# Kernel optimization log

Measured on AMD Instinct MI355X. Metric: run time of the kernel, lower is better.

## Reference

```python
import jax, jax.numpy as jnp
import numpy as np

IMG = 1024       # original image resolution implied by (1024 - 1) normalization
STRIDE = 16
TEMP = 0.1
EPS = 1e-12      # F.normalize eps


def setup_inputs() -> dict:
    key = jax.random.key(0)
    k1, k2, k3, k4, k5 = jax.random.split(key, 5)
    B, C, Hf, Wf, N = 32, 256, 64, 64, 128
    feats_src = jax.random.normal(k1, (B, C, Hf, Wf), dtype=jnp.float32)
    feats_trg = jax.random.normal(k2, (B, C, Hf, Wf), dtype=jnp.float32)
    kps_src = jax.random.uniform(k3, (B, N, 2), dtype=jnp.float32) * (IMG - 1)
    kps_trg = jax.random.uniform(k4, (B, N, 2), dtype=jnp.float32) * (IMG - 1)
    kps_mask = jax.random.randint(k5, (B, N), 0, 2, dtype=jnp.int32)
    return {"feats_src": feats_src, "feats_trg": feats_trg,
            "kps_src": kps_src, "kps_trg": kps_trg, "kps_mask": kps_mask}


def _l2norm_c(x):
    # F.normalize(x, dim=1): x / max(||x||_2, eps) along channel dim
    n = jnp.sqrt(jnp.sum(x * x, axis=1, keepdims=True))
    return x / jnp.maximum(n, EPS)


def _bilinear_sample(feats, kps):
    # feats: [B,C,Hf,Wf]; kps: [B,N,2] pixel coords in [0, IMG-1]
    # Equivalent to F.grid_sample(align_corners=True, bilinear) with
    # grid = kps/(IMG-1)*2-1 -> pixel coords kps/(IMG-1)*(size-1).
    B, C, Hf, Wf = feats.shape
    x = kps[..., 0] / (IMG - 1) * (Wf - 1)  # [B,N]
    y = kps[..., 1] / (IMG - 1) * (Hf - 1)
    x0 = jnp.clip(jnp.floor(x), 0, Wf - 1).astype(jnp.int32)
    y0 = jnp.clip(jnp.floor(y), 0, Hf - 1).astype(jnp.int32)
    x1 = jnp.clip(x0 + 1, 0, Wf - 1)
    y1 = jnp.clip(y0 + 1, 0, Hf - 1)
    fx = x - x0.astype(x.dtype)
    fy = y - y0.astype(y.dtype)
    ft = jnp.transpose(feats, (0, 2, 3, 1))      # [B,Hf,Wf,C]
    bb = jnp.arange(B)[:, None]                  # [B,1] broadcasts to [B,N]
    g = lambda yy, xx: ft[bb, yy, xx]            # [B,N,C]
    wa = ((1 - fx) * (1 - fy))[..., None]
    wb = ((1 - fx) * fy)[..., None]
    wc = (fx * (1 - fy))[..., None]
    wd = (fx * fy)[..., None]
    return wa * g(y0, x0) + wb * g(y1, x0) + wc * g(y0, x1) + wd * g(y1, x1)


def reference(feats_src, feats_trg, kps_src, kps_trg, kps_mask):
    B, C, Hf, Wf = feats_src.shape
    N = kps_src.shape[1]
    fs = _l2norm_c(feats_src)
    ftg = _l2norm_c(feats_trg)

    # Query features sampled at source keypoints: [B,N,C]
    q = _bilinear_sample(fs, kps_src)

    # Logits over all target spatial positions: [B,N,Hf*Wf]
    trg_flat = ftg.reshape(B, C, Hf * Wf)
    logits = jnp.einsum('bnc,bcm->bnm', q, trg_flat) / TEMP

    # Bilinear soft targets at target keypoints (feature-grid coords)
    gx = kps_trg[..., 0] / STRIDE
    gy = kps_trg[..., 1] / STRIDE
    x0 = jnp.clip(jnp.floor(gx), 0, Wf - 1).astype(jnp.int32)
    x1 = jnp.clip(x0 + 1, 0, Wf - 1)
    y0 = jnp.clip(jnp.floor(gy), 0, Hf - 1).astype(jnp.int32)
    y1 = jnp.clip(y0 + 1, 0, Hf - 1)
    x0f, x1f = x0.astype(gx.dtype), x1.astype(gx.dtype)
    y0f, y1f = y0.astype(gy.dtype), y1.astype(gy.dtype)
    wa = (x1f - gx) * (y1f - gy)
    wb = (x1f - gx) * (gy - y0f)
    wc = (gx - x0f) * (y1f - gy)
    wd = (gx - x0f) * (gy - y0f)

    m = (kps_mask != 0).astype(logits.dtype)     # [B,N]
    w = jnp.stack([wa, wb, wc, wd], axis=-1) * m[..., None]   # [B,N,4]
    idx = jnp.stack([y0 * Wf + x0, y1 * Wf + x0,
                     y0 * Wf + x1, y1 * Wf + x1], axis=-1)    # [B,N,4]
    bb = jnp.arange(B)[:, None, None]
    nn = jnp.arange(N)[None, :, None]
    soft_targets = jnp.zeros_like(logits).at[bb, nn, idx].add(w)

    log_probs = jax.nn.log_softmax(logits, axis=-1)
    loss = -(soft_targets * log_probs).sum(axis=-1)           # [B,N]
    denom = jnp.maximum(m.sum(), 1.0)
    return (loss * m).sum() / denom
```

## Files before the change

### kernel.cpp

```cpp
#include <hip/hip_runtime.h>
#include <math.h>

#define B_    32
#define C_    256
#define HF    64
#define WF    64
#define M_    4096
#define N_    128
#define IMGM1 1023.0f
#define TEMP_ 0.1f
#define EPS_  1e-12f
#define NCH   32
#define SAS   40

typedef __attribute__((ext_vector_type(8))) short short8;
typedef __attribute__((ext_vector_type(4))) float floatx4;

__device__ __forceinline__ unsigned short f2bf(float x) {
  unsigned int u = __float_as_uint(x);
  u += 0x7fffu + ((u >> 16) & 1u);
  return (unsigned short)(u >> 16);
}
__device__ __forceinline__ float bf2f(unsigned short h) {
  return __uint_as_float(((unsigned int)h) << 16);
}
__device__ __forceinline__ float wave_sum(float v) {
#pragma unroll
  for (int off = 32; off; off >>= 1) v += __shfl_down(v, off, 64);
  return v;
}

__device__ __forceinline__ void src_geom(float kx, float ky, int& x0, int& y0,
                                         int& x1, int& y1, float& fx, float& fy) {
  const float x = kx / IMGM1 * (float)(WF - 1);
  const float y = ky / IMGM1 * (float)(HF - 1);
  x0 = (int)fminf(fmaxf(floorf(x), 0.f), 63.f);
  y0 = (int)fminf(fmaxf(floorf(y), 0.f), 63.f);
  x1 = min(x0 + 1, 63);
  y1 = min(y0 + 1, 63);
  fx = x - (float)x0;
  fy = y - (float)y0;
}

__global__ __launch_bounds__(256) void k1a_stage(const float* __restrict__ fs,
                                                 const float* __restrict__ kps,
                                                 ushort* __restrict__ corner,
                                                 float* __restrict__ ssqg) {
  const int cg = blockIdx.x, b = blockIdx.y, t = threadIdx.x;
  const int c0 = cg * 2;
  __shared__ __align__(16) float plane[2 * M_];
  __shared__ float4 ssq2[256];

  const float4* src = (const float4*)(fs + ((size_t)(b * C_ + c0)) * M_);
  float4* dst = (float4*)plane;
#pragma unroll
  for (int i = 0; i < 8; i++) dst[t + 256 * i] = src[t + 256 * i];
  __syncthreads();

  const int n = t & 127, p = t >> 7;
  const int c = c0 + p;
  const float kx = kps[((size_t)b * N_ + n) * 2 + 0];
  const float ky = kps[((size_t)b * N_ + n) * 2 + 1];
  int x0, y0, x1, y1; float fx, fy;
  src_geom(kx, ky, x0, y0, x1, y1, fx, fy);

  const float* pl = plane + p * M_;
  const float f00 = pl[y0 * WF + x0];
  const float f10 = pl[y1 * WF + x0];
  const float f01 = pl[y0 * WF + x1];
  const float f11 = pl[y1 * WF + x1];

  ushort4 cr;
  cr.x = f2bf(f00); cr.y = f2bf(f10); cr.z = f2bf(f01); cr.w = f2bf(f11);
  *(ushort4*)&corner[(((size_t)b * C_ + c) * N_ + n) * 4] = cr;

  ssq2[t] = make_float4(f00 * f00, f10 * f10, f01 * f01, f11 * f11);
  __syncthreads();
  if (t < 128) {
    const float4 a = ssq2[t], bq = ssq2[t + 128];
    float* g = ssqg + ((size_t)b * N_ + t) * 4;
    atomicAdd(g + 0, a.x + bq.x);
    atomicAdd(g + 1, a.y + bq.y);
    atomicAdd(g + 2, a.z + bq.z);
    atomicAdd(g + 3, a.w + bq.w);
  }
}

__global__ __launch_bounds__(256) void k1b_combine(const ushort* __restrict__ corner,
                                                   const float* __restrict__ ssqg,
                                                   const float* __restrict__ kps,
                                                   ushort* __restrict__ qbf) {
  const int n = blockIdx.x, b = blockIdx.y, c = threadIdx.x;
  const float kx = kps[((size_t)b * N_ + n) * 2 + 0];
  const float ky = kps[((size_t)b * N_ + n) * 2 + 1];
  int x0, y0, x1, y1; float fx, fy;
  src_geom(kx, ky, x0, y0, x1, y1, fx, fy);
  const float wa = (1.f - fx) * (1.f - fy), wb = (1.f - fx) * fy;
  const float wc = fx * (1.f - fy), wd = fx * fy;

  const float4 sq = *(const float4*)&ssqg[((size_t)b * N_ + n) * 4];
  const float r0 = 1.f / fmaxf(sqrtf(sq.x), EPS_);
  const float r1 = 1.f / fmaxf(sqrtf(sq.y), EPS_);
  const float r2 = 1.f / fmaxf(sqrtf(sq.z), EPS_);
  const float r3 = 1.f / fmaxf(sqrtf(sq.w), EPS_);

  const ushort4 cr = *(const ushort4*)&corner[(((size_t)b * C_ + c) * N_ + n) * 4];
  const float qv = wa * bf2f(cr.x) * r0 + wb * bf2f(cr.y) * r1 +
                   wc * bf2f(cr.z) * r2 + wd * bf2f(cr.w) * r3;
  qbf[((size_t)b * N_ + n) * C_ + c] = f2bf(qv);
}

__global__ __launch_bounds__(256) void k2_mfma(const float* __restrict__ trg,
                                               const ushort* __restrict__ qbf,
                                               const float* __restrict__ kps_trg,
                                               const int* __restrict__ mask,
                                               float2* __restrict__ part,
                                               float* __restrict__ tacc) {
  const int t = threadIdx.x;
  const int mb = blockIdx.x, b = blockIdx.y;
  const int m0 = mb * 128;
  const int wave = t >> 6, lane = t & 63;
  const int wn = wave >> 1, wm = wave & 1;
  const int lg = lane >> 4, ln = lane & 15;

  __shared__ __align__(16) short sA[128 * SAS];
  __shared__ __align__(16) short sB[128 * SAS];
  __shared__ __align__(16) float ssqp[16 * 128];
  __shared__ float scl[128];
  __shared__ float2 lser[128 * 2];
  __shared__ __align__(16) int   tidx[128][4];
  __shared__ __align__(16) float tw[128][4];

  floatx4 acc[4][4];
#pragma unroll
  for (int i = 0; i < 4; i++)
#pragma unroll
    for (int j = 0; j < 4; j++) acc[i][j] = (floatx4)0.f;

  float ssq[8];
#pragma unroll
  for (int e = 0; e < 8; e++) ssq[e] = 0.f;

  const ushort* qb = qbf + (size_t)b * N_ * C_;
  const float*  tb = trg + (size_t)b * C_ * M_ + m0;
  const int kk  = 2 * (t >> 4);
  const int m8  = (t & 15) * 8;
  const int gB  = kk >> 3;
  const int kin = kk & 7;

  for (int k0 = 0; k0 < C_; k0 += 32) {
#pragma unroll
    for (int l2 = 0; l2 < 2; l2++) {
      const int flat = t + 256 * l2;
      const int an = flat >> 2, ag = flat & 3;
      const short8 v = *(const short8*)(qb + an * C_ + k0 + ag * 8);
      *(short8*)&sA[an * SAS + ag * 8] = v;
    }
    {
      const float* p0 = tb + (size_t)(k0 + kk) * M_ + m8;
      const float* p1 = p0 + M_;
      const float4 a0 = *(const float4*)p0, a1 = *(const float4*)(p0 + 4);
      const float4 b0 = *(const float4*)p1, b1 = *(const float4*)(p1 + 4);
      const float v0[8] = {a0.x, a0.y, a0.z, a0.w, a1.x, a1.y, a1.z, a1.w};
      const float v1[8] = {b0.x, b0.y, b0.z, b0.w, b1.x, b1.y, b1.z, b1.w};
#pragma unroll
      for (int e = 0; e < 8; e++) {
        ssq[e] += v0[e] * v0[e] + v1[e] * v1[e];
        const int m = m8 + e;
        const int fm = (m >> 3) & 3;
        const unsigned int pr = (unsigned int)f2bf(v0[e]) | ((unsigned int)f2bf(v1[e]) << 16);
        *(unsigned int*)&sB[m * SAS + ((gB ^ fm) << 3) + kin] = pr;
      }
    }
    __syncthreads();
    short8 af[4], bfr[4];
#pragma unroll
    for (int i = 0; i < 4; i++)
      af[i] = *(const short8*)&sA[(wn * 64 + i * 16 + ln) * SAS + (lg << 3)];
#pragma unroll
    for (int j = 0; j < 4; j++) {
      const int m = wm * 64 + j * 16 + ln;
      const int fm = (m >> 3) & 3;
      bfr[j] = *(const short8*)&sB[m * SAS + ((lg ^ fm) << 3)];
    }
#pragma unroll
    for (int i = 0; i < 4; i++)
#pragma unroll
      for (int j = 0; j < 4; j++)
        acc[i][j] = __builtin_amdgcn_mfma_f32_16x16x32_bf16(af[i], bfr[j], acc[i][j], 0, 0, 0);
    __syncthreads();
  }

  *(float4*)&ssqp[(t >> 4) * 128 + m8]     = make_float4(ssq[0], ssq[1], ssq[2], ssq[3]);
  *(float4*)&ssqp[(t >> 4) * 128 + m8 + 4] = make_float4(ssq[4], ssq[5], ssq[6], ssq[7]);
  __syncthreads();
  if (t < 128) {
    float s = 0.f;
#pragma unroll
    for (int g = 0; g < 16; g++) s += ssqp[g * 128 + t];
    scl[t] = 1.f / (fmaxf(sqrtf(s), EPS_) * TEMP_);
    const float kx = kps_trg[((size_t)b * N_ + t) * 2 + 0];
    const float ky = kps_trg[((size_t)b * N_ + t) * 2 + 1];
    const float gx = kx * (1.f / 16.f), gy = ky * (1.f / 16.f);
    const int x0 = (int)fminf(fmaxf(floorf(gx), 0.f), 63.f);
    const int y0 = (int)fminf(fmaxf(floorf(gy), 0.f), 63.f);
    const int x1 = min(x0 + 1, 63), y1 = min(y0 + 1, 63);
    const float x0f = (float)x0, x1f = (float)x1, y0f = (float)y0, y1f = (float)y1;
    const float mk = (mask[(size_t)b * N_ + t] != 0) ? 1.f : 0.f;
    tidx[t][0] = y0 * WF + x0; tw[t][0] = (x1f - gx) * (y1f - gy) * mk;
    tidx[t][1] = y1 * WF + x0; tw[t][1] = (x1f - gx) * (gy - y0f) * mk;
    tidx[t][2] = y0 * WF + x1; tw[t][2] = (gx - x0f) * (y1f - gy) * mk;
    tidx[t][3] = y1 * WF + x1; tw[t][3] = (gx - x0f) * (gy - y0f) * mk;
  }
  __syncthreads();

  float scj[4];
#pragma unroll
  for (int j = 0; j < 4; j++) scj[j] = scl[wm * 64 + j * 16 + ln];
#pragma unroll
  for (int i = 0; i < 4; i++)
#pragma unroll
    for (int j = 0; j < 4; j++) acc[i][j] *= scj[j];

#pragma unroll
  for (int i = 0; i < 4; i++) {
#pragma unroll
    for (int r = 0; r < 4; r++) {
      float mx = fmaxf(fmaxf(acc[i][0][r], acc[i][1][r]), fmaxf(acc[i][2][r], acc[i][3][r]));
#pragma unroll
      for (int msk = 1; msk < 16; msk <<= 1) mx = fmaxf(mx, __shfl_xor(mx, msk, 64));
      float sm = __expf(acc[i][0][r] - mx) + __expf(acc[i][1][r] - mx) +
                 __expf(acc[i][2][r] - mx) + __expf(acc[i][3][r] - mx);
#pragma unroll
      for (int msk = 1; msk < 16; msk <<= 1) sm += __shfl_xor(sm, msk, 64);
      if (ln == 0) lser[(wn * 64 + i * 16 + lg * 4 + r) * 2 + wm] = make_float2(mx, sm);

      const int n = wn * 64 + i * 16 + lg * 4 + r;
      const int4  id4 = *(const int4*)&tidx[n][0];
      const float4 w4 = *(const float4*)&tw[n][0];
      const int   ida[4] = {id4.x, id4.y, id4.z, id4.w};
      const float wwa[4] = {w4.x, w4.y, w4.z, w4.w};
#pragma unroll
      for (int j = 0; j < 4; j++) {
        const int mg = m0 + wm * 64 + j * 16 + ln;
        const float lv = acc[i][j][r];
#pragma unroll
        for (int cc = 0; cc < 4; cc++)
          if (ida[cc] == mg && wwa[cc] != 0.f)
            atomicAdd(&tacc[(size_t)b * N_ + n], wwa[cc] * lv);
      }
    }
  }
  __syncthreads();
  if (t < 128) {
    const float2 u = lser[t * 2 + 0], v = lser[t * 2 + 1];
    const float M = fmaxf(u.x, v.x);
    const float S = u.y * __expf(u.x - M) + v.y * __expf(v.x - M);
    part[((size_t)b * N_ + t) * NCH + mb] = make_float2(M, S);
  }
}

__global__ __launch_bounds__(128) void k4_comb(const float2* __restrict__ part,
                                               const float* __restrict__ tacc,
                                               const float* __restrict__ kps_trg,
                                               const int* __restrict__ mask,
                                               float* __restrict__ gs) {
  const int b = blockIdx.x, t = threadIdx.x;
  const float2* p = part + ((size_t)b * N_ + t) * NCH;
  float M = -INFINITY;
#pragma unroll 8
  for (int c = 0; c < NCH; c++) M = fmaxf(M, p[c].x);
  float S = 0.f;
#pragma unroll 8
  for (int c = 0; c < NCH; c++) S += p[c].y * __expf(p[c].x - M);
  const float lse = M + logf(S);

  const float kx = kps_trg[((size_t)b * N_ + t) * 2 + 0];
  const float ky = kps_trg[((size_t)b * N_ + t) * 2 + 1];
  const float gx = kx * (1.f / 16.f), gy = ky * (1.f / 16.f);
  const int x0 = (int)fminf(fmaxf(floorf(gx), 0.f), 63.f);
  const int y0 = (int)fminf(fmaxf(floorf(gy), 0.f), 63.f);
  const int x1 = min(x0 + 1, 63), y1 = min(y0 + 1, 63);
  const float mk = (mask[(size_t)b * N_ + t] != 0) ? 1.f : 0.f;
  const float wsum = (float)(x1 - x0) * (float)(y1 - y0) * mk;

  float loss = wsum * lse - tacc[(size_t)b * N_ + t];
  float cnt = mk;
  loss = wave_sum(loss);
  cnt = wave_sum(cnt);
  __shared__ float sl[2], sc2[2];
  if ((t & 63) == 0) { sl[t >> 6] = loss; sc2[t >> 6] = cnt; }
  __syncthreads();
  if (t == 0) {
    atomicAdd(&gs[0], sl[0] + sl[1]);
    atomicAdd(&gs[1], sc2[0] + sc2[1]);
  }
}

__global__ void k5_final(const float* __restrict__ gs, float* __restrict__ out) {
  out[0] = gs[0] / fmaxf(gs[1], 1.f);
}

extern "C" void kernel_launch(void* const* d_in, const int* in_sizes, int n_in,
                              void* d_out, int out_size, void* d_ws, size_t ws_size,
                              hipStream_t stream) {
  const float* feats_src = (const float*)d_in[0];
  const float* feats_trg = (const float*)d_in[1];
  const float* kps_src   = (const float*)d_in[2];
  const float* kps_trg   = (const float*)d_in[3];
  const int*   kps_mask  = (const int*)d_in[4];
  float* out = (float*)d_out;

  char* wsb = (char*)d_ws;
  float*  ssqg   = (float*)(wsb + 0);
  float*  tacc   = (float*)(wsb + 65536);
  float*  gs     = (float*)(wsb + 81920);
  ushort* corner = (ushort*)(wsb + 82432);
  ushort* qbf    = (ushort*)(wsb + 8471040);
  float2* part   = (float2*)(wsb + 10568192);

  hipMemsetAsync(wsb, 0, 81928, stream);

  k1a_stage<<<dim3(C_ / 2, B_), 256, 0, stream>>>(feats_src, kps_src, corner, ssqg);
  k1b_combine<<<dim3(N_, B_), 256, 0, stream>>>(corner, ssqg, kps_src, qbf);
  k2_mfma<<<dim3(NCH, B_), 256, 0, stream>>>(feats_trg, qbf, kps_trg, kps_mask, part, tacc);
  k4_comb<<<dim3(B_), 128, 0, stream>>>(part, tacc, kps_trg, kps_mask, gs);
  k5_final<<<1, 1, 0, stream>>>(gs, out);
}
```

Baseline: 347.5 us.

## Coalesce combine kernel via LDS transpose and skip irrelevant target-scatter checks

The combine kernel now processes 32 channels by all 128 keypoints per block. It precomputes the per-keypoint weight times inverse norm once in shared memory, reads corner data contiguously, and transposes through LDS so the bf16 query writes go out as coalesced ushort4 stores instead of strided per-channel reads. The MFMA kernel also builds a per-keypoint bitmask of which 128-column chunks hold nonzero target corners, so warps skip the compare and atomic loop for chunks they cannot touch. This costs extra shared memory and a sync, and it assumes the 4096/128 = 32 chunks fit in a 32-bit mask.

```diff
diff --git a/kernel.cpp b/kernel.cpp
--- a/kernel.cpp
+++ b/kernel.cpp
@@ -86,28 +86,54 @@
   }
 }
 
-__global__ __launch_bounds__(256) void k1b_combine(const ushort* __restrict__ corner,
-                                                   const float* __restrict__ ssqg,
-                                                   const float* __restrict__ kps,
-                                                   ushort* __restrict__ qbf) {
-  const int n = blockIdx.x, b = blockIdx.y, c = threadIdx.x;
-  const float kx = kps[((size_t)b * N_ + n) * 2 + 0];
-  const float ky = kps[((size_t)b * N_ + n) * 2 + 1];
-  int x0, y0, x1, y1; float fx, fy;
-  src_geom(kx, ky, x0, y0, x1, y1, fx, fy);
-  const float wa = (1.f - fx) * (1.f - fy), wb = (1.f - fx) * fy;
-  const float wc = fx * (1.f - fy), wd = fx * fy;
-
-  const float4 sq = *(const float4*)&ssqg[((size_t)b * N_ + n) * 4];
-  const float r0 = 1.f / fmaxf(sqrtf(sq.x), EPS_);
-  const float r1 = 1.f / fmaxf(sqrtf(sq.y), EPS_);
-  const float r2 = 1.f / fmaxf(sqrtf(sq.z), EPS_);
-  const float r3 = 1.f / fmaxf(sqrtf(sq.w), EPS_);
-
-  const ushort4 cr = *(const ushort4*)&corner[(((size_t)b * C_ + c) * N_ + n) * 4];
-  const float qv = wa * bf2f(cr.x) * r0 + wb * bf2f(cr.y) * r1 +
-                   wc * bf2f(cr.z) * r2 + wd * bf2f(cr.w) * r3;
-  qbf[((size_t)b * N_ + n) * C_ + c] = f2bf(qv);
+__global__ __launch_bounds__(256) void k1b2_combine(const ushort* __restrict__ corner,
+                                                    const float* __restrict__ ssqg,
+                                                    const float* __restrict__ kps,
+                                                    ushort* __restrict__ qbf) {
+  const int cg = blockIdx.x, b = blockIdx.y, t = threadIdx.x;
+  __shared__ float4 uw[128];
+  __shared__ ushort sQ[32][137];
+
+  if (t < 128) {
+    const int n = t;
+    const float kx = kps[((size_t)b * N_ + n) * 2 + 0];
+    const float ky = kps[((size_t)b * N_ + n) * 2 + 1];
+    int x0, y0, x1, y1; float fx, fy;
+    src_geom(kx, ky, x0, y0, x1, y1, fx, fy);
+    const float wa = (1.f - fx) * (1.f - fy), wb = (1.f - fx) * fy;
+    const float wc = fx * (1.f - fy), wd = fx * fy;
+    const float4 sq = *(const float4*)&ssqg[((size_t)b * N_ + n) * 4];
+    const float r0 = 1.f / fmaxf(sqrtf(sq.x), EPS_);
+    const float r1 = 1.f / fmaxf(sqrtf(sq.y), EPS_);
+    const float r2 = 1.f / fmaxf(sqrtf(sq.z), EPS_);
+    const float r3 = 1.f / fmaxf(sqrtf(sq.w), EPS_);
+    uw[n] = make_float4(wa * r0, wb * r1, wc * r2, wd * r3);
+  }
+  __syncthreads();
+
+  const ushort* cb = corner + (((size_t)b * C_ + cg * 32) * N_) * 4;
+#pragma unroll
+  for (int i = 0; i < 16; i++) {
+    const int e = t + 256 * i;
+    const int n = e & 127, cl = e >> 7;
+    const ushort4 cr = *(const ushort4*)&cb[((size_t)cl * N_ + n) * 4];
+    const float4 u = uw[n];
+    const float qv = u.x * bf2f(cr.x) + u.y * bf2f(cr.y) +
+                     u.z * bf2f(cr.z) + u.w * bf2f(cr.w);
+    sQ[cl][n] = f2bf(qv);
+  }
+  __syncthreads();
+
+  ushort* qb = qbf + (size_t)b * N_ * C_ + cg * 32;
+#pragma unroll
+  for (int i = 0; i < 4; i++) {
+    const int o = t + 256 * i;
+    const int n = o >> 3, c4 = (o & 7) * 4;
+    ushort4 w4;
+    w4.x = sQ[c4 + 0][n]; w4.y = sQ[c4 + 1][n];
+    w4.z = sQ[c4 + 2][n]; w4.w = sQ[c4 + 3][n];
+    *(ushort4*)&qb[(size_t)n * C_ + c4] = w4;
+  }
 }
 
 __global__ __launch_bounds__(256) void k2_mfma(const float* __restrict__ trg,
@@ -130,6 +156,7 @@
   __shared__ float2 lser[128 * 2];
   __shared__ __align__(16) int   tidx[128][4];
   __shared__ __align__(16) float tw[128][4];
+  __shared__ unsigned tmask[128];
 
   floatx4 acc[4][4];
 #pragma unroll
@@ -207,10 +234,22 @@
     const int x1 = min(x0 + 1, 63), y1 = min(y0 + 1, 63);
     const float x0f = (float)x0, x1f = (float)x1, y0f = (float)y0, y1f = (float)y1;
     const float mk = (mask[(size_t)b * N_ + t] != 0) ? 1.f : 0.f;
-    tidx[t][0] = y0 * WF + x0; tw[t][0] = (x1f - gx) * (y1f - gy) * mk;
-    tidx[t][1] = y1 * WF + x0; tw[t][1] = (x1f - gx) * (gy - y0f) * mk;
-    tidx[t][2] = y0 * WF + x1; tw[t][2] = (gx - x0f) * (y1f - gy) * mk;
-    tidx[t][3] = y1 * WF + x1; tw[t][3] = (gx - x0f) * (gy - y0f) * mk;
+    const int i0 = y0 * WF + x0, i1 = y1 * WF + x0;
+    const int i2 = y0 * WF + x1, i3 = y1 * WF + x1;
+    const float w0 = (x1f - gx) * (y1f - gy) * mk;
+    const float w1 = (x1f - gx) * (gy - y0f) * mk;
+    const float w2 = (gx - x0f) * (y1f - gy) * mk;
+    const float w3 = (gx - x0f) * (gy - y0f) * mk;
+    tidx[t][0] = i0; tw[t][0] = w0;
+    tidx[t][1] = i1; tw[t][1] = w1;
+    tidx[t][2] = i2; tw[t][2] = w2;
+    tidx[t][3] = i3; tw[t][3] = w3;
+    unsigned tm = 0u;
+    if (w0 != 0.f) tm |= 1u << (i0 >> 7);
+    if (w1 != 0.f) tm |= 1u << (i1 >> 7);
+    if (w2 != 0.f) tm |= 1u << (i2 >> 7);
+    if (w3 != 0.f) tm |= 1u << (i3 >> 7);
+    tmask[t] = tm;
   }
   __syncthreads();
 
@@ -222,6 +261,7 @@
 #pragma unroll
     for (int j = 0; j < 4; j++) acc[i][j] *= scj[j];
 
+  const unsigned mbbit = 1u << mb;
 #pragma unroll
   for (int i = 0; i < 4; i++) {
 #pragma unroll
@@ -236,18 +276,20 @@
       if (ln == 0) lser[(wn * 64 + i * 16 + lg * 4 + r) * 2 + wm] = make_float2(mx, sm);
 
       const int n = wn * 64 + i * 16 + lg * 4 + r;
-      const int4  id4 = *(const int4*)&tidx[n][0];
-      const float4 w4 = *(const float4*)&tw[n][0];
-      const int   ida[4] = {id4.x, id4.y, id4.z, id4.w};
-      const float wwa[4] = {w4.x, w4.y, w4.z, w4.w};
-#pragma unroll
-      for (int j = 0; j < 4; j++) {
-        const int mg = m0 + wm * 64 + j * 16 + ln;
-        const float lv = acc[i][j][r];
-#pragma unroll
-        for (int cc = 0; cc < 4; cc++)
-          if (ida[cc] == mg && wwa[cc] != 0.f)
-            atomicAdd(&tacc[(size_t)b * N_ + n], wwa[cc] * lv);
+      if (tmask[n] & mbbit) {
+        const int4  id4 = *(const int4*)&tidx[n][0];
+        const float4 w4 = *(const float4*)&tw[n][0];
+        const int   ida[4] = {id4.x, id4.y, id4.z, id4.w};
+        const float wwa[4] = {w4.x, w4.y, w4.z, w4.w};
+#pragma unroll
+        for (int j = 0; j < 4; j++) {
+          const int mg = m0 + wm * 64 + j * 16 + ln;
+          const float lv = acc[i][j][r];
+#pragma unroll
+          for (int cc = 0; cc < 4; cc++)
+            if (ida[cc] == mg && wwa[cc] != 0.f)
+              atomicAdd(&tacc[(size_t)b * N_ + n], wwa[cc] * lv);
+        }
       }
     }
   }
@@ -322,7 +364,7 @@
   hipMemsetAsync(wsb, 0, 81928, stream);
 
   k1a_stage<<<dim3(C_ / 2, B_), 256, 0, stream>>>(feats_src, kps_src, corner, ssqg);
-  k1b_combine<<<dim3(N_, B_), 256, 0, stream>>>(corner, ssqg, kps_src, qbf);
+  k1b2_combine<<<dim3(C_ / 32, B_), 256, 0, stream>>>(corner, ssqg, kps_src, qbf);
   k2_mfma<<<dim3(NCH, B_), 256, 0, stream>>>(feats_trg, qbf, kps_trg, kps_mask, part, tacc);
   k4_comb<<<dim3(B_), 128, 0, stream>>>(part, tacc, kps_trg, kps_mask, gs);
   k5_final<<<1, 1, 0, stream>>>(gs, out);
```

Result: faster. 327.4 us (-5.8%).
